# Kernel tuning notes

Measured on AMD Instinct MI355X. Metric: run time of the kernel, lower is better.

Reference implementation:

```python
import jax, jax.numpy as jnp
import numpy as np

B, S, D, P = 4, 2048, 1024, 1024

def setup_inputs() -> dict:
    key = jax.random.key(0)
    k1, k2, k3, k4 = jax.random.split(key, 4)
    x = jax.random.normal(k1, (B, S, D), dtype=jnp.float32)
    # nn.Linear weight is (out, in); store transposed (in, out) for x @ W
    scale = 1.0 / np.sqrt(D)
    Wq = jax.random.normal(k2, (D, P), dtype=jnp.float32) * scale
    Wk = jax.random.normal(k3, (D, P), dtype=jnp.float32) * scale
    Wv = jax.random.normal(k4, (D, P), dtype=jnp.float32) * scale
    return {"x": x, "Wq": Wq, "Wk": Wk, "Wv": Wv}

def reference(x, Wq, Wk, Wv):
    # projections (no bias)
    q = x @ Wq  # (B,S,P)
    k = x @ Wk
    v = x @ Wv
    scores = jnp.einsum('bsd,btd->bst', q, k)  # (B,S,S)
    seq = x.shape[1]
    causal = jnp.triu(jnp.ones((seq, seq), dtype=bool), k=1)
    scores = jnp.where(causal, -jnp.inf, scores)
    scores = scores / jnp.sqrt(jnp.asarray(P, dtype=scores.dtype))
    attn = jax.nn.softmax(scores, axis=-1)
    # dropout_prob=0.0 -> identity
    context = jnp.einsum('bst,btd->bsd', attn, v)  # (B,S,P)
    return context
```

## Files before the change

### kernel.cpp

```cpp
#include <hip/hip_runtime.h>
#include <hip/hip_bf16.h>


#define BDIM 4
#define SDIM 2048
#define DDIM 1024
#define PDIM 1024

typedef __attribute__((ext_vector_type(8))) short bf16x8;
typedef __attribute__((ext_vector_type(4))) float f32x4;

__device__ __forceinline__ unsigned short f2bf(float f) {
    union { float f; unsigned int u; } v; v.f = f;
    unsigned int u = v.u;
    unsigned int r = (u + 0x7fffu + ((u >> 16) & 1u)) >> 16;
    return (unsigned short)r;
}

__device__ __forceinline__ float bf2f(unsigned short h) {
    union { unsigned int u; float f; } v;
    v.u = ((unsigned int)h) << 16;
    return v.f;
}

__device__ __forceinline__ void async16(const unsigned short* g, unsigned short* l) {
    __builtin_amdgcn_global_load_lds(
        (const __attribute__((address_space(1))) unsigned int*)g,
        (__attribute__((address_space(3))) unsigned int*)l,
        16, 0, 0);
}

__device__ __forceinline__ void storeC(float* C, size_t idx, float v) { C[idx] = v; }
__device__ __forceinline__ void storeC(unsigned short* C, size_t idx, float v) { C[idx] = f2bf(v); }

__global__ __launch_bounds__(256) void prep_kernel(const float* __restrict__ x,
                                                   const float* __restrict__ W0,
                                                   const float* __restrict__ W1,
                                                   const float* __restrict__ W2,
                                                   unsigned short* __restrict__ Xb,
                                                   unsigned short* __restrict__ WT) {
    int bid = blockIdx.x;
    if (bid < 4096) {
        size_t i = (size_t)bid * 256 + threadIdx.x;
        float4 a = ((const float4*)x)[2 * i];
        float4 b = ((const float4*)x)[2 * i + 1];
        bf16x8 o;
        o[0] = (short)f2bf(a.x); o[1] = (short)f2bf(a.y);
        o[2] = (short)f2bf(a.z); o[3] = (short)f2bf(a.w);
        o[4] = (short)f2bf(b.x); o[5] = (short)f2bf(b.y);
        o[6] = (short)f2bf(b.z); o[7] = (short)f2bf(b.w);
        ((bf16x8*)Xb)[i] = o;
    } else {
        int idx = bid - 4096;
        int wz = idx >> 10;
        int t = idx & 1023;
        const float* W = (wz == 0) ? W0 : (wz == 1) ? W1 : W2;
        unsigned short* Tz = WT + (size_t)wz * DDIM * PDIM;
        __shared__ float tle[32][33];
        int c0 = (t & 31) * 32, r0 = (t >> 5) * 32;
        int tx = threadIdx.x & 31, ty = threadIdx.x >> 5;
        for (int i = ty; i < 32; i += 8)
            tle[i][tx] = W[(size_t)(r0 + i) * PDIM + c0 + tx];
        __syncthreads();
        for (int i = ty; i < 32; i += 8)
            Tz[(size_t)(c0 + i) * DDIM + r0 + tx] = f2bf(tle[tx][i]);
    }
}

template <int LDA, int LDB, int LDC, int KMAX, int MODE, typename CT>
__global__ __launch_bounds__(256) void gemm_bt(
    const unsigned short* __restrict__ A0, const unsigned short* __restrict__ A1,
    long long sA,
    const unsigned short* __restrict__ B0, long long sB,
    CT* __restrict__ C0, CT* __restrict__ C1, long long sC,
    unsigned short* __restrict__ Kb, unsigned short* __restrict__ VT,
    float alpha) {
    const int BM = 128, BN = 128, BK = 64;
    const int ABUF = BM * BK;
    __shared__ __attribute__((aligned(16))) unsigned short smem[2 * ABUF + BN * BK];
    unsigned short* BsBuf = smem + 2 * ABUF;

    int tm, tn;
    if (MODE == 1) {
        int i = blockIdx.x;
        int t = (int)((sqrtf(8.f * i + 1.f) - 1.f) * 0.5f);
        if ((t + 1) * (t + 2) / 2 <= i) t++;
        if (t * (t + 1) / 2 > i) t--;
        tm = t * BM;
        tn = (i - t * (t + 1) / 2) * BN;
    } else if (MODE == 2) {
        tm = ((int)gridDim.y - 1 - (int)blockIdx.y) * BM;
        tn = blockIdx.x * BN;
    } else {
        tm = blockIdx.y * BM;
        tn = blockIdx.x * BN;
    }
    int kend = (MODE == 2) ? min(KMAX, tm + BM) : KMAX;

    int z = blockIdx.z;
    const unsigned short* A = (z < 2 ? A0 : A1) + (long long)(z & 1) * sA;
    const unsigned short* Bt = B0 + (long long)z * sB;
    CT* C = (z < 2 ? C0 : C1) + (long long)(z & 1) * sC;

    int tid  = threadIdx.x;
    int lane = tid & 63;
    int wave = tid >> 6;
    int wr   = (wave >> 1) * 64;
    int wc   = (wave & 1) * 64;
    int quad = lane >> 4;
    int l16  = lane & 15;
    int rsw  = l16 & 7;

    f32x4 acc[4][4] = {};

    int srow = tid >> 3;
    int scol = ((tid & 7) ^ (srow & 7)) * 8;
    const unsigned short* Ag = A + (size_t)(tm + srow) * LDA + scol;
    const unsigned short* Bg = Bt + (size_t)(tn + srow) * LDB + scol;

    auto issueA = [&](int k0, int buf) {
        unsigned short* la = smem + buf * ABUF + tid * 8;
        async16(Ag + k0, la);
        async16(Ag + k0 + 32 * LDA, la + 2048);
        async16(Ag + k0 + 64 * LDA, la + 4096);
        async16(Ag + k0 + 96 * LDA, la + 6144);
    };
    auto issueB = [&](int k0) {
        unsigned short* lb = BsBuf + tid * 8;
        async16(Bg + k0, lb);
        async16(Bg + k0 + 32 * LDB, lb + 2048);
        async16(Bg + k0 + 64 * LDB, lb + 4096);
        async16(Bg + k0 + 96 * LDB, lb + 6144);
    };

    auto kbody = [&](int i, int ns) {
        __syncthreads();
        bf16x8 bf[2][4];
#pragma unroll
        for (int s = 0; s < 2; s++)
#pragma unroll
            for (int j = 0; j < 4; j++)
                bf[s][j] = *(const bf16x8*)(BsBuf + (wc + j * 16 + l16) * BK
                                                  + ((s * 4 + quad) ^ rsw) * 8);
        __syncthreads();
        if (i + 1 < ns) { issueA((i + 1) * BK, (i + 1) & 1); issueB((i + 1) * BK); }
        const unsigned short* As = smem + (i & 1) * ABUF;
#pragma unroll
        for (int s = 0; s < 2; s++) {
            int chunk = ((s * 4 + quad) ^ rsw) * 8;
            bf16x8 af[4];
#pragma unroll
            for (int ii = 0; ii < 4; ii++)
                af[ii] = *(const bf16x8*)(As + (wr + ii * 16 + l16) * BK + chunk);
#pragma unroll
            for (int ii = 0; ii < 4; ii++)
#pragma unroll
                for (int j = 0; j < 4; j++)
                    acc[ii][j] = __builtin_amdgcn_mfma_f32_16x16x32_bf16(
                        af[ii], bf[s][j], acc[ii][j], 0, 0, 0);
        }
    };

    issueA(0, 0);
    issueB(0);
    if constexpr (MODE != 2) {
        constexpr int NS = KMAX / BK;
#pragma unroll
        for (int i = 0; i < NS; i++) kbody(i, NS);
    } else {
        int ns = kend / BK;
        for (int i = 0; i < ns; i++) kbody(i, ns);
    }

    if constexpr (MODE == 0) {
        if (tn < 2048) {
            unsigned short* D = (tn < 1024 ? (unsigned short*)C0 : Kb);
            int cbase = tn & 1023;
#pragma unroll
            for (int i = 0; i < 4; i++) {
                int r0 = tm + wr + i * 16 + quad * 4;
#pragma unroll
                for (int j = 0; j < 4; j++) {
                    int c = cbase + wc + j * 16 + l16;
#pragma unroll
                    for (int rr = 0; rr < 4; rr++)
                        D[(size_t)(r0 + rr) * 1024 + c] = f2bf(acc[i][j][rr]);
                }
            }
        } else {
            int b = tm >> 11;
            int s0 = tm & 2047;
            unsigned short* VTb = VT + (size_t)b * (PDIM * SDIM)
                                     + (size_t)(tn - 2048) * SDIM + s0;
            const int TP = 136;
            unsigned short* T = smem;
            __syncthreads();
#pragma unroll
            for (int p = 0; p < 4; p++) {
                int jbase = -1;
                if (wc == 0 && p == 0) jbase = 0;
                if (wc == 0 && p == 1) jbase = 2;
                if (wc == 64 && p == 2) jbase = 0;
                if (wc == 64 && p == 3) jbase = 2;
                if (jbase >= 0) {
#pragma unroll
                    for (int jj = 0; jj < 2; jj++) {
                        int j = jbase + jj;
                        int c = (wc + j * 16 + l16) - 32 * p;
#pragma unroll
                        for (int i = 0; i < 4; i++) {
                            int r = wr + i * 16 + quad * 4;
                            ushort4 w;
                            w.x = f2bf(acc[i][j][0]); w.y = f2bf(acc[i][j][1]);
                            w.z = f2bf(acc[i][j][2]); w.w = f2bf(acc[i][j][3]);
                            *(ushort4*)(T + c * TP + r) = w;
                        }
                    }
                }
                __syncthreads();
                {
                    int lr = tid >> 3;
                    int ck = (tid & 7) * 16;
                    bf16x8 u0 = *(const bf16x8*)(T + lr * TP + ck);
                    bf16x8 u1 = *(const bf16x8*)(T + lr * TP + ck + 8);
                    unsigned short* dst = VTb + (size_t)(32 * p + lr) * SDIM + ck;
                    *(bf16x8*)(dst) = u0;
                    *(bf16x8*)(dst + 8) = u1;
                }
                __syncthreads();
            }
        }
    } else {
#pragma unroll
        for (int i = 0; i < 4; i++) {
            int r0 = tm + wr + i * 16 + quad * 4;
#pragma unroll
            for (int j = 0; j < 4; j++) {
                int c = tn + wc + j * 16 + l16;
#pragma unroll
                for (int rr = 0; rr < 4; rr++) {
                    int r = r0 + rr;
                    if (MODE == 1 && c > r) continue;
                    storeC(C, (size_t)r * LDC + c, acc[i][j][rr] * alpha);
                }
            }
        }
    }
}

__global__ __launch_bounds__(256) void softmax_causal(unsigned short* __restrict__ S01,
                                                      unsigned short* __restrict__ S23,
                                                      long long sS) {
    int row = blockIdx.x;
    int b = blockIdx.y;
    unsigned short* srow = (b < 2 ? S01 : S23) + (long long)(b & 1) * sS + (size_t)row * SDIM;
    int tid = threadIdx.x;
    int j0 = tid * 8;
    int valid = row + 1;
    int bound = ((row >> 7) + 1) << 7;
    bool active = j0 < valid;
    __shared__ float red[4];

    float f[8];
    if (active) {
        bf16x8 v8 = *(const bf16x8*)(srow + j0);
#pragma unroll
        for (int i = 0; i < 8; i++) f[i] = bf2f((unsigned short)v8[i]);
    }

    float m = -1e30f;
    if (active) {
#pragma unroll
        for (int i = 0; i < 8; i++) if (j0 + i < valid) m = fmaxf(m, f[i]);
    }
#pragma unroll
    for (int o = 32; o; o >>= 1) m = fmaxf(m, __shfl_xor(m, o, 64));
    if ((tid & 63) == 0) red[tid >> 6] = m;
    __syncthreads();
    m = fmaxf(fmaxf(red[0], red[1]), fmaxf(red[2], red[3]));
    __syncthreads();

    float e[8] = {0.f, 0.f, 0.f, 0.f, 0.f, 0.f, 0.f, 0.f};
    float l = 0.f;
    if (active) {
#pragma unroll
        for (int i = 0; i < 8; i++) {
            e[i] = (j0 + i < valid) ? __expf(f[i] - m) : 0.f;
            l += e[i];
        }
    }
#pragma unroll
    for (int o = 32; o; o >>= 1) l += __shfl_xor(l, o, 64);
    if ((tid & 63) == 0) red[tid >> 6] = l;
    __syncthreads();
    l = red[0] + red[1] + red[2] + red[3];
    float inv = 1.0f / l;

    if (j0 < bound) {
        bf16x8 o8;
#pragma unroll
        for (int i = 0; i < 8; i++) o8[i] = (short)f2bf(e[i] * inv);
        *(bf16x8*)(srow + j0) = o8;
    }
}

extern "C" void kernel_launch(void* const* d_in, const int* in_sizes, int n_in,
                              void* d_out, int out_size, void* d_ws, size_t ws_size,
                              hipStream_t stream) {
    const float* x  = (const float*)d_in[0];
    const float* Wq = (const float*)d_in[1];
    const float* Wk = (const float*)d_in[2];
    const float* Wv = (const float*)d_in[3];
    float* out = (float*)d_out;

    const size_t MS = (size_t)BDIM * SDIM;
    const long long SS = (long long)SDIM * SDIM;
    char* ws = (char*)d_ws;
    size_t off = 0;
    unsigned short* Xb   = (unsigned short*)(ws + off);
    unsigned short* S01  = Xb;                          off += MS * DDIM * 2;
    unsigned short* WT   = (unsigned short*)(ws + off); off += 3ull * DDIM * PDIM * 2;
    unsigned short* Q    = (unsigned short*)(ws + off); off += MS * PDIM * 2;
    unsigned short* Kb   = (unsigned short*)(ws + off); off += MS * PDIM * 2;
    unsigned short* VT   = (unsigned short*)(ws + off); off += MS * PDIM * 2;
    unsigned short* S23  = (unsigned short*)(ws + off); off += 2ull * SS * 2;

    prep_kernel<<<4096 + 3072, 256, 0, stream>>>(x, Wq, Wk, Wv, Xb, WT);

    gemm_bt<DDIM, DDIM, PDIM, DDIM, 0, unsigned short>
        <<<dim3(3 * PDIM / 128, MS / 128, 1), 256, 0, stream>>>(
        Xb, Xb, 0, WT, 0, Q, Q, 0, Kb, VT, 1.0f);

    const long long sQ = (long long)SDIM * PDIM;
    const float alpha = 1.0f / 32.0f;

    gemm_bt<PDIM, PDIM, SDIM, PDIM, 1, unsigned short>
        <<<dim3(136, 1, BDIM), 256, 0, stream>>>(
        Q, Q + 2 * sQ, sQ, Kb, sQ, S01, S23, SS, nullptr, nullptr, alpha);

    softmax_causal<<<dim3(SDIM, BDIM), 256, 0, stream>>>(S01, S23, SS);

    const long long sOut = (long long)SDIM * PDIM;
    gemm_bt<SDIM, SDIM, PDIM, SDIM, 2, float>
        <<<dim3(PDIM / 128, SDIM / 128, BDIM), 256, 0, stream>>>(
        S01, S23, SS, VT, sQ, out, out + 2 * sOut, sOut, nullptr, nullptr, 1.0f);
}
```

Measured before the change: 228.2 us.

## Add 256x256-tile QKV projection kernel with 8 waves and swizzled LDS

Replaces the 128x128 MODE-0 GEMM for the fused QKV projection with a dedicated 512-thread kernel using 256x256 tiles, XOR-swizzled LDS, double-buffered async loads, and interleaved read/MFMA phases with barriers and setprio. The larger tile is meant to raise arithmetic intensity and MFMA utilisation for the projection. The MODE-2 PV GEMM also reverses the row order only for the first two batches, to balance the causal-length tail across the grid. The cost is a large LDS footprint (128KB) and high register pressure, which limit occupancy.

```diff
diff --git a/kernel.cpp b/kernel.cpp
--- a/kernel.cpp
+++ b/kernel.cpp
@@ -67,6 +67,173 @@
     }
 }
 
+__global__ __launch_bounds__(512, 2) void qkv256(
+    const unsigned short* __restrict__ Xb,
+    const unsigned short* __restrict__ WT,
+    unsigned short* __restrict__ Q,
+    unsigned short* __restrict__ Kb,
+    unsigned short* __restrict__ VT) {
+    const int BK = 64;
+    const int TILE = 256 * BK;
+    __shared__ __attribute__((aligned(16))) unsigned short smem[4 * TILE];
+
+    int tm = blockIdx.y * 256;
+    int tn = blockIdx.x * 256;
+
+    int tid  = threadIdx.x;
+    int lane = tid & 63;
+    int wave = tid >> 6;
+    int wr   = (wave >> 2) * 128;
+    int wc   = (wave & 3) * 64;
+    int quad = lane >> 4;
+    int l16  = lane & 15;
+    int rsw  = l16 & 7;
+
+    f32x4 acc[8][4] = {};
+
+    int srow = tid >> 3;
+    int scol = ((tid & 7) ^ (srow & 7)) * 8;
+    const unsigned short* Ag = Xb + (size_t)(tm + srow) * DDIM + scol;
+    const unsigned short* Bg = WT + (size_t)(tn + srow) * DDIM + scol;
+
+    auto issueTile = [&](int k0, int buf) {
+        unsigned short* la = smem + buf * (2 * TILE) + tid * 8;
+        unsigned short* lb = la + TILE;
+#pragma unroll
+        for (int p = 0; p < 4; p++) {
+            async16(Ag + k0 + p * 64 * DDIM, la + p * 4096);
+            async16(Bg + k0 + p * 64 * DDIM, lb + p * 4096);
+        }
+    };
+
+    auto readA = [&](bf16x8 (&af)[4][2], const unsigned short* As, int mq) {
+#pragma unroll
+        for (int i2 = 0; i2 < 4; i2++)
+#pragma unroll
+            for (int s = 0; s < 2; s++)
+                af[i2][s] = *(const bf16x8*)(As + (wr + mq * 64 + i2 * 16 + l16) * BK
+                                                + ((s * 4 + quad) ^ rsw) * 8);
+    };
+    auto readB = [&](bf16x8 (&bfq)[2][2], const unsigned short* Bs, int nq) {
+#pragma unroll
+        for (int j2 = 0; j2 < 2; j2++)
+#pragma unroll
+            for (int s = 0; s < 2; s++)
+                bfq[j2][s] = *(const bf16x8*)(Bs + (wc + nq * 32 + j2 * 16 + l16) * BK
+                                                 + ((s * 4 + quad) ^ rsw) * 8);
+    };
+    auto mfmaQ = [&](const bf16x8 (&af)[4][2], const bf16x8 (&bfq)[2][2],
+                     int mq, int nq) {
+        __builtin_amdgcn_s_setprio(1);
+#pragma unroll
+        for (int s = 0; s < 2; s++)
+#pragma unroll
+            for (int i2 = 0; i2 < 4; i2++)
+#pragma unroll
+                for (int j2 = 0; j2 < 2; j2++)
+                    acc[mq * 4 + i2][nq * 2 + j2] =
+                        __builtin_amdgcn_mfma_f32_16x16x32_bf16(
+                            af[i2][s], bfq[j2][s], acc[mq * 4 + i2][nq * 2 + j2],
+                            0, 0, 0);
+        __builtin_amdgcn_s_setprio(0);
+    };
+
+    const int nt = DDIM / BK;
+    issueTile(0, 0);
+    issueTile(BK, 1);
+    asm volatile("s_waitcnt vmcnt(8)" ::: "memory");
+    asm volatile("s_barrier" ::: "memory");
+
+#pragma unroll 2
+    for (int t = 0; t < nt; t++) {
+        const unsigned short* As = smem + (t & 1) * (2 * TILE);
+        const unsigned short* Bs = As + TILE;
+        bf16x8 af[4][2];
+        bf16x8 bfq[2][2];
+
+        readA(af, As, 0);
+        readB(bfq, Bs, 0);
+        asm volatile("s_barrier" ::: "memory");
+        mfmaQ(af, bfq, 0, 0);
+
+        readB(bfq, Bs, 1);
+        asm volatile("s_barrier" ::: "memory");
+        mfmaQ(af, bfq, 0, 1);
+
+        readA(af, As, 1);
+        asm volatile("s_barrier" ::: "memory");
+        mfmaQ(af, bfq, 1, 1);
+
+        readB(bfq, Bs, 0);
+        asm volatile("s_barrier" ::: "memory");
+        mfmaQ(af, bfq, 1, 0);
+
+        asm volatile("s_barrier" ::: "memory");
+        if (t + 2 < nt) {
+            issueTile((t + 2) * BK, t & 1);
+            asm volatile("s_waitcnt vmcnt(8)" ::: "memory");
+            asm volatile("s_barrier" ::: "memory");
+        } else if (t + 1 < nt) {
+            asm volatile("s_waitcnt vmcnt(0)" ::: "memory");
+            asm volatile("s_barrier" ::: "memory");
+        }
+    }
+
+    if (tn < 2048) {
+        unsigned short* D = (tn < 1024) ? Q : Kb;
+        int cbase = tn & 1023;
+#pragma unroll
+        for (int i = 0; i < 8; i++) {
+            int r0 = tm + wr + (i >> 2) * 64 + (i & 3) * 16 + quad * 4;
+#pragma unroll
+            for (int j = 0; j < 4; j++) {
+                int c = cbase + wc + (j >> 1) * 32 + (j & 1) * 16 + l16;
+#pragma unroll
+                for (int rr = 0; rr < 4; rr++)
+                    D[(size_t)(r0 + rr) * 1024 + c] = f2bf(acc[i][j][rr]);
+            }
+        }
+    } else {
+        int b = tm >> 11;
+        int s0 = tm & 2047;
+        int vbase = tn - 2048;
+        unsigned short* VTb = VT + (size_t)b * (PDIM * SDIM)
+                                 + (size_t)vbase * SDIM + s0;
+        const int TP = 264;
+        unsigned short* T = smem;
+#pragma unroll
+        for (int sl = 0; sl < 8; sl++) {
+            if ((wave & 3) == (sl >> 1)) {
+                int jb = (sl & 1) * 2;
+#pragma unroll
+                for (int jj = 0; jj < 2; jj++) {
+                    int j = jb + jj;
+                    int cl = jj * 16 + l16;
+#pragma unroll
+                    for (int i = 0; i < 8; i++) {
+                        int rl = wr + (i >> 2) * 64 + (i & 3) * 16 + quad * 4;
+                        ushort4 w;
+                        w.x = f2bf(acc[i][j][0]); w.y = f2bf(acc[i][j][1]);
+                        w.z = f2bf(acc[i][j][2]); w.w = f2bf(acc[i][j][3]);
+                        *(ushort4*)(T + cl * TP + rl) = w;
+                    }
+                }
+            }
+            __syncthreads();
+            {
+                int cl = tid >> 4;
+                int sc = (tid & 15) * 16;
+                bf16x8 u0 = *(const bf16x8*)(T + cl * TP + sc);
+                bf16x8 u1 = *(const bf16x8*)(T + cl * TP + sc + 8);
+                unsigned short* dst = VTb + (size_t)(sl * 32 + cl) * SDIM + sc;
+                *(bf16x8*)dst = u0;
+                *(bf16x8*)(dst + 8) = u1;
+            }
+            __syncthreads();
+        }
+    }
+}
+
 template <int LDA, int LDB, int LDC, int KMAX, int MODE, typename CT>
 __global__ __launch_bounds__(256) void gemm_bt(
     const unsigned short* __restrict__ A0, const unsigned short* __restrict__ A1,
@@ -89,7 +256,9 @@
         tm = t * BM;
         tn = (i - t * (t + 1) / 2) * BN;
     } else if (MODE == 2) {
-        tm = ((int)gridDim.y - 1 - (int)blockIdx.y) * BM;
+        int yy = (blockIdx.z < 2) ? ((int)gridDim.y - 1 - (int)blockIdx.y)
+                                  : (int)blockIdx.y;
+        tm = yy * BM;
         tn = blockIdx.x * BN;
     } else {
         tm = blockIdx.y * BM;
@@ -172,77 +341,17 @@
         for (int i = 0; i < ns; i++) kbody(i, ns);
     }
 
-    if constexpr (MODE == 0) {
-        if (tn < 2048) {
-            unsigned short* D = (tn < 1024 ? (unsigned short*)C0 : Kb);
-            int cbase = tn & 1023;
-#pragma unroll
-            for (int i = 0; i < 4; i++) {
-                int r0 = tm + wr + i * 16 + quad * 4;
-#pragma unroll
-                for (int j = 0; j < 4; j++) {
-                    int c = cbase + wc + j * 16 + l16;
-#pragma unroll
-                    for (int rr = 0; rr < 4; rr++)
-                        D[(size_t)(r0 + rr) * 1024 + c] = f2bf(acc[i][j][rr]);
-                }
-            }
-        } else {
-            int b = tm >> 11;
-            int s0 = tm & 2047;
-            unsigned short* VTb = VT + (size_t)b * (PDIM * SDIM)
-                                     + (size_t)(tn - 2048) * SDIM + s0;
-            const int TP = 136;
-            unsigned short* T = smem;
-            __syncthreads();
-#pragma unroll
-            for (int p = 0; p < 4; p++) {
-                int jbase = -1;
-                if (wc == 0 && p == 0) jbase = 0;
-                if (wc == 0 && p == 1) jbase = 2;
-                if (wc == 64 && p == 2) jbase = 0;
-                if (wc == 64 && p == 3) jbase = 2;
-                if (jbase >= 0) {
-#pragma unroll
-                    for (int jj = 0; jj < 2; jj++) {
-                        int j = jbase + jj;
-                        int c = (wc + j * 16 + l16) - 32 * p;
-#pragma unroll
-                        for (int i = 0; i < 4; i++) {
-                            int r = wr + i * 16 + quad * 4;
-                            ushort4 w;
-                            w.x = f2bf(acc[i][j][0]); w.y = f2bf(acc[i][j][1]);
-                            w.z = f2bf(acc[i][j][2]); w.w = f2bf(acc[i][j][3]);
-                            *(ushort4*)(T + c * TP + r) = w;
-                        }
-                    }
-                }
-                __syncthreads();
-                {
-                    int lr = tid >> 3;
-                    int ck = (tid & 7) * 16;
-                    bf16x8 u0 = *(const bf16x8*)(T + lr * TP + ck);
-                    bf16x8 u1 = *(const bf16x8*)(T + lr * TP + ck + 8);
-                    unsigned short* dst = VTb + (size_t)(32 * p + lr) * SDIM + ck;
-                    *(bf16x8*)(dst) = u0;
-                    *(bf16x8*)(dst + 8) = u1;
-                }
-                __syncthreads();
-            }
-        }
-    } else {
-#pragma unroll
-        for (int i = 0; i < 4; i++) {
-            int r0 = tm + wr + i * 16 + quad * 4;
-#pragma unroll
-            for (int j = 0; j < 4; j++) {
-                int c = tn + wc + j * 16 + l16;
-#pragma unroll
-                for (int rr = 0; rr < 4; rr++) {
-                    int r = r0 + rr;
-                    if (MODE == 1 && c > r) continue;
-                    storeC(C, (size_t)r * LDC + c, acc[i][j][rr] * alpha);
-                }
+#pragma unroll
+    for (int i = 0; i < 4; i++) {
+        int r0 = tm + wr + i * 16 + quad * 4;
+#pragma unroll
+        for (int j = 0; j < 4; j++) {
+            int c = tn + wc + j * 16 + l16;
+#pragma unroll
+            for (int rr = 0; rr < 4; rr++) {
+                int r = r0 + rr;
+                if (MODE == 1 && c > r) continue;
+                storeC(C, (size_t)r * LDC + c, acc[i][j][rr] * alpha);
             }
         }
     }
@@ -327,9 +436,7 @@
 
     prep_kernel<<<4096 + 3072, 256, 0, stream>>>(x, Wq, Wk, Wv, Xb, WT);
 
-    gemm_bt<DDIM, DDIM, PDIM, DDIM, 0, unsigned short>
-        <<<dim3(3 * PDIM / 128, MS / 128, 1), 256, 0, stream>>>(
-        Xb, Xb, 0, WT, 0, Q, Q, 0, Kb, VT, 1.0f);
+    qkv256<<<dim3(3 * PDIM / 256, MS / 256, 1), 512, 0, stream>>>(Xb, WT, Q, Kb, VT);
 
     const long long sQ = (long long)SDIM * PDIM;
     const float alpha = 1.0f / 32.0f;
```

After: 241.4 us. +5.8%, slower.
